# Optimization experiments

Measured on AMD Instinct MI355X. Metric: run time of the kernel, lower is better.

## Reference

```python
import jax, jax.numpy as jnp
import numpy as np
import math

B, S, D = 8, 4096, 768
H = 12
DH = D // H  # attention_head_size = 64


def setup_inputs() -> dict:
    key = jax.random.key(0)
    ks = jax.random.split(key, 6)
    sc = 0.02
    return {
        "hidden_states": jax.random.normal(ks[0], (B, S, D), dtype=jnp.float32),
        "attention_mask": jnp.zeros((B, 1, S), dtype=jnp.float32),
        "Wq": jax.random.normal(ks[1], (D, D), dtype=jnp.float32) * sc,
        "bq": jnp.zeros((D,), dtype=jnp.float32),
        "Wqa": jax.random.normal(ks[2], (H, D), dtype=jnp.float32) * sc,
        "bqa": jnp.zeros((H,), dtype=jnp.float32),
        "Wk": jax.random.normal(ks[3], (D, D), dtype=jnp.float32) * sc,
        "bk": jnp.zeros((D,), dtype=jnp.float32),
        "Wt": jax.random.normal(ks[4], (D, D), dtype=jnp.float32) * sc,
        "bt": jnp.zeros((D,), dtype=jnp.float32),
    }


def reference(hidden_states, attention_mask, Wq, bq, Wqa, bqa, Wk, bk, Wt, bt):
    inv_sqrt_dh = 1.0 / math.sqrt(DH)
    # projections (torch nn.Linear: x @ W.T + b)
    q = hidden_states @ Wq.T + bq            # [B,S,D]
    k = hidden_states @ Wk.T + bk            # [B,S,D]
    # query attention logits -> [B,H,S]
    qfs = jnp.swapaxes(q @ Wqa.T + bqa, 1, 2) * inv_sqrt_dh + attention_mask
    qw = jax.nn.softmax(qfs, axis=-1)        # [B,H,S]
    ql = jnp.swapaxes(q.reshape(B, S, H, DH), 1, 2)  # [B,H,S,DH]
    kl = jnp.swapaxes(k.reshape(B, S, H, DH), 1, 2)  # [B,H,S,DH]
    # global pooled query per head
    pooled_q = jnp.einsum('bhs,bhsd->bhd', qw, ql)   # [B,H,DH]
    # key attention over pooled query
    qks = jnp.einsum('bhsd,bhd->bhs', kl, pooled_q) * inv_sqrt_dh + attention_mask
    qkw = jax.nn.softmax(qks, axis=-1)       # [B,H,S]
    pooled_k = jnp.einsum('bhs,bhsd->bhd', qkw, kl)  # [B,H,DH]
    # gate query with pooled key, merge heads
    wv = pooled_k[:, :, None, :] * ql        # [B,H,S,DH]
    wv = jnp.swapaxes(wv, 1, 2).reshape(B, S, D)
    return wv @ Wt.T + bt + q
```

## Files before the change

### kernel.cpp

```cpp
#include <hip/hip_runtime.h>
#include <cstdint>
#include <cstddef>

#define S_LEN 4096
#define NB 8
#define NH 12
#define DMODEL 768
#define DHEAD 64
#define M_TOT (NB * S_LEN)
#define INV_SQRT_DH 0.125f
#define WSZ (DMODEL * DMODEL)

typedef __attribute__((ext_vector_type(4))) float f32x4;
typedef __attribute__((ext_vector_type(8))) short bf16x8;

__device__ inline float bf2f(unsigned short h) {
    union { unsigned int u; float f; } v; v.u = ((unsigned int)h) << 16; return v.f;
}
__device__ inline unsigned short f2bf(float f) {
    union { float f; unsigned int u; } v; v.f = f;
    unsigned int r = v.u + 0x7FFFu + ((v.u >> 16) & 1u);
    return (unsigned short)(r >> 16);
}

__device__ inline void gload_lds16(const unsigned short* gp, void* lp) {
    __builtin_amdgcn_global_load_lds((const __attribute__((address_space(1))) void*)gp,
                                     (__attribute__((address_space(3))) void*)lp,
                                     16, 0, 0);
}

__global__ void prep_all(const float* __restrict__ hs,
                         const float* __restrict__ Wq, const float* __restrict__ Wk,
                         const float* __restrict__ Wt, const float* __restrict__ Wqa,
                         const float* __restrict__ bq, const float* __restrict__ bk,
                         unsigned short* __restrict__ hs_bf,
                         unsigned short* __restrict__ Wqk_bf, unsigned short* __restrict__ Wt_bf,
                         unsigned short* __restrict__ Wqa_bf, float* __restrict__ bqk) {
    int bid = blockIdx.x;
    int t = threadIdx.x;
    if (bid < 24576) {
        int off = bid * 1024 + t * 4;
        float4 v = *(const float4*)(hs + off);
        ushort4 o;
        o.x = f2bf(v.x); o.y = f2bf(v.y); o.z = f2bf(v.z); o.w = f2bf(v.w);
        *(ushort4*)(hs_bf + off) = o;
        return;
    }
    bid -= 24576;
    if (bid < 1728) {
        const float* src = (bid < 576) ? Wq : ((bid < 1152) ? Wk : Wt);
        unsigned short* dst = (bid < 576) ? Wqk_bf : ((bid < 1152) ? (Wqk_bf + WSZ) : Wt_bf);
        int off = (bid % 576) * 1024 + t * 4;
        float4 v = *(const float4*)(src + off);
        ushort4 o;
        o.x = f2bf(v.x); o.y = f2bf(v.y); o.z = f2bf(v.z); o.w = f2bf(v.w);
        *(ushort4*)(dst + off) = o;
    } else if (bid < 1740) {
        int off = (bid - 1728) * 1024 + t * 4;
        int h = off / DMODEL;
        ushort4 o = {0, 0, 0, 0};
        if (h < NH) {
            float4 v = *(const float4*)(Wqa + off);
            o.x = f2bf(v.x); o.y = f2bf(v.y); o.z = f2bf(v.z); o.w = f2bf(v.w);
        }
        *(ushort4*)(Wqa_bf + off) = o;
    } else {
        int off = (bid - 1740) * 1024 + t * 4;
        if (off < 2 * DMODEL) {
            const float* src = (off < DMODEL) ? (bq + off) : (bk + off - DMODEL);
            *(float4*)(bqk + off) = *(const float4*)src;
        }
    }
}

#define PH_MID() do { __builtin_amdgcn_s_barrier(); \
    asm volatile("s_waitcnt lgkmcnt(0)"); \
    __builtin_amdgcn_sched_barrier(0); \
    __builtin_amdgcn_s_setprio(1); } while (0)
#define PH_END() do { __builtin_amdgcn_s_setprio(0); \
    __builtin_amdgcn_s_barrier(); } while (0)

#define STG_A(q, kt, BO) gload_lds16(pA + (size_t)((q) * 64) * 768 + (kt) * 64, \
                                     lds + (BO) + (q) * 8192 + wOff)
#define STG_B(q, kt, BO) gload_lds16(pB + (size_t)((q) * 64) * 768 + (kt) * 64, \
                                     lds + (BO) + 32768 + (q) * 8192 + wOff)

#define LD_A(mh, BO) do { _Pragma("unroll") for (int mm = 0; mm < 4; ++mm) { \
    a[mm][0] = *(const bf16x8*)(lds + (BO) + aRd0 + ((mh) * 4 + mm) * 2048); \
    a[mm][1] = *(const bf16x8*)(lds + (BO) + aRd1 + ((mh) * 4 + mm) * 2048); } } while (0)
#define LD_B(nh, BO) do { _Pragma("unroll") for (int nn = 0; nn < 2; ++nn) { \
    b[(nh) * 2 + nn][0] = *(const bf16x8*)(lds + (BO) + bRd0 + ((nh) * 2 + nn) * 2048); \
    b[(nh) * 2 + nn][1] = *(const bf16x8*)(lds + (BO) + bRd1 + ((nh) * 2 + nn) * 2048); } } while (0)
#define MFMAQ(mh, nh) do { _Pragma("unroll") for (int mm = 0; mm < 4; ++mm) \
    _Pragma("unroll") for (int nn = 0; nn < 2; ++nn) { \
        acc[(mh) * 4 + mm][(nh) * 2 + nn] = __builtin_amdgcn_mfma_f32_16x16x32_bf16( \
            a[mm][0], b[(nh) * 2 + nn][0], acc[(mh) * 4 + mm][(nh) * 2 + nn], 0, 0, 0); \
        acc[(mh) * 4 + mm][(nh) * 2 + nn] = __builtin_amdgcn_mfma_f32_16x16x32_bf16( \
            a[mm][1], b[(nh) * 2 + nn][1], acc[(mh) * 4 + mm][(nh) * 2 + nn], 0, 0, 0); } } while (0)

__global__ __launch_bounds__(512, 2) void gemm8(
    const unsigned short* __restrict__ A,
    const unsigned short* __restrict__ Bw,
    const float* __restrict__ bias,
    unsigned short* __restrict__ qOut,
    unsigned short* __restrict__ kOut,
    int ntn)
{
    __shared__ __align__(16) char lds[131072];

    int nwg = gridDim.x;
    int bid = blockIdx.x;
    int cpx = nwg >> 3;
    int swz = (bid & 7) * cpx + (bid >> 3);
    int bidn = swz % ntn, bidm = swz / ntn;
    int m0 = bidm * 256, n0 = bidn * 256;

    int t = threadIdx.x;
    int w = t >> 6, lane = t & 63;
    int lr = lane & 15, lk = lane >> 4;
    int wr = w >> 2, wc = w & 3;
    int wOff = w << 10;

    int srow = t >> 3;
    int sblk = (t & 7) ^ (srow & 7);
    const unsigned short* pA = A + (size_t)(m0 + srow) * 768 + sblk * 8;
    const unsigned short* pB = Bw + (size_t)(n0 + srow) * 768 + sblk * 8;

    int sx = lr & 7;
    int aRd0 = (wr * 128 + lr) * 128 + ((0 + lk) ^ sx) * 16;
    int aRd1 = (wr * 128 + lr) * 128 + ((4 + lk) ^ sx) * 16;
    int bRd0 = 32768 + (wc * 64 + lr) * 128 + ((0 + lk) ^ sx) * 16;
    int bRd1 = 32768 + (wc * 64 + lr) * 128 + ((4 + lk) ^ sx) * 16;

    f32x4 acc[8][4];
#pragma unroll
    for (int m = 0; m < 8; ++m)
#pragma unroll
        for (int n = 0; n < 4; ++n)
            acc[m][n] = (f32x4){0.f, 0.f, 0.f, 0.f};
    bf16x8 a[4][2], b[4][2];

    STG_A(0, 0, 0); STG_A(1, 0, 0); STG_A(2, 0, 0); STG_A(3, 0, 0);
    STG_B(0, 0, 0); STG_B(1, 0, 0); STG_B(2, 0, 0); STG_B(3, 0, 0);
    STG_A(0, 1, 65536); STG_A(2, 1, 65536);
    STG_B(0, 1, 65536); STG_B(1, 1, 65536); STG_B(2, 1, 65536); STG_B(3, 1, 65536);
    asm volatile("s_waitcnt vmcnt(6)");
    __builtin_amdgcn_s_barrier();

    for (int i = 0; i < 6; ++i) {
        int ktE = 2 * i, ktO = 2 * i + 1;
        int s2 = (i < 5);
        LD_A(0, 0); LD_B(0, 0);
        STG_A(1, ktO, 65536); STG_A(3, ktO, 65536);
        PH_MID(); MFMAQ(0, 0); PH_END();
        LD_B(1, 0);
        if (s2) { STG_A(0, ktE + 2, 0); STG_A(2, ktE + 2, 0); }
        PH_MID(); MFMAQ(0, 1); PH_END();
        LD_A(1, 0);
        if (s2) { STG_B(0, ktE + 2, 0); STG_B(1, ktE + 2, 0); }
        PH_MID(); MFMAQ(1, 1); PH_END();
        if (s2) { STG_B(2, ktE + 2, 0); STG_B(3, ktE + 2, 0); }
        PH_MID(); MFMAQ(1, 0);
        __builtin_amdgcn_s_setprio(0);
        if (s2) { asm volatile("s_waitcnt vmcnt(6)"); }
        else    { asm volatile("s_waitcnt vmcnt(0)"); }
        __builtin_amdgcn_s_barrier();
        LD_A(0, 65536); LD_B(0, 65536);
        if (s2) { STG_A(1, ktE + 2, 0); STG_A(3, ktE + 2, 0); }
        PH_MID(); MFMAQ(0, 0); PH_END();
        LD_B(1, 65536);
        if (s2) { STG_A(0, ktO + 2, 65536); STG_A(2, ktO + 2, 65536); }
        PH_MID(); MFMAQ(0, 1); PH_END();
        LD_A(1, 65536);
        if (s2) { STG_B(0, ktO + 2, 65536); STG_B(1, ktO + 2, 65536); }
        PH_MID(); MFMAQ(1, 1); PH_END();
        if (s2) { STG_B(2, ktO + 2, 65536); STG_B(3, ktO + 2, 65536); }
        PH_MID(); MFMAQ(1, 0);
        __builtin_amdgcn_s_setprio(0);
        if (s2) { asm volatile("s_waitcnt vmcnt(6)"); }
        __builtin_amdgcn_s_barrier();
    }

    unsigned short* outBf = (bidn < 3) ? qOut : kOut;
    int nc0 = (bidn < 3) ? n0 : (n0 - 768);
#pragma unroll
    for (int m = 0; m < 8; ++m) {
        int gr0 = m0 + wr * 128 + m * 16 + lk * 4;
#pragma unroll
        for (int n = 0; n < 4; ++n) {
            int gc = n0 + wc * 64 + n * 16 + lr;
            int oc = nc0 + wc * 64 + n * 16 + lr;
            float bv = bias[gc];
#pragma unroll
            for (int r = 0; r < 4; ++r) {
                int gr = gr0 + r;
                outBf[(size_t)gr * 768 + oc] = f2bf(acc[m][n][r] + bv);
            }
        }
    }
}

#define STG6_A(q, kt, SB) gload_lds16(pA + (size_t)((q) * 64) * 768 + (kt) * 64, \
                                      lds + (SB) + (q) * 8192 + wOff)
#define STG6_B(q, kt, SB) gload_lds16(pB + (size_t)((q) * 64) * 768 + (kt) * 64, \
                                      lds + (SB) + 32768 + (q) * 8192 + wOff)

__global__ __launch_bounds__(512, 2) void gemm3(
    const unsigned short* __restrict__ A,
    const unsigned short* __restrict__ W8,
    const float* __restrict__ bias,
    float* __restrict__ outF,
    const unsigned short* __restrict__ resid)
{
    __shared__ __align__(16) char lds[147456];

    int nwg = gridDim.x;
    int bid = blockIdx.x;
    int cpx = nwg >> 3;
    int swz = (bid & 7) * cpx + (bid >> 3);
    int bidn = swz % 6, bidm = swz / 6;
    int m0 = bidm * 256, n0 = bidn * 128;

    const unsigned short* Bw = W8 + (size_t)(m0 >> 12) * WSZ;

    int t = threadIdx.x;
    int w = t >> 6, lane = t & 63;
    int lr = lane & 15, lk = lane >> 4;
    int wr = w >> 1, wc = w & 1;
    int wOff = w << 10;

    int srow = t >> 3;
    int sblk = (t & 7) ^ (srow & 7);
    const unsigned short* pA = A + (size_t)(m0 + srow) * 768 + sblk * 8;
    const unsigned short* pB = Bw + (size_t)(n0 + srow) * 768 + sblk * 8;

    int sx = lr & 7;
    int aRd0 = (wr * 64 + lr) * 128 + ((0 + lk) ^ sx) * 16;
    int aRd1 = (wr * 64 + lr) * 128 + ((4 + lk) ^ sx) * 16;
    int bRd0 = 32768 + (wc * 64 + lr) * 128 + ((0 + lk) ^ sx) * 16;
    int bRd1 = 32768 + (wc * 64 + lr) * 128 + ((4 + lk) ^ sx) * 16;

    f32x4 acc[4][4];
#pragma unroll
    for (int m = 0; m < 4; ++m)
#pragma unroll
        for (int n = 0; n < 4; ++n)
            acc[m][n] = (f32x4){0.f, 0.f, 0.f, 0.f};
    bf16x8 a[4][2], b[4][2];

    STG6_A(0, 0, 0); STG6_A(1, 0, 0); STG6_A(2, 0, 0); STG6_A(3, 0, 0);
    STG6_B(0, 0, 0); STG6_B(1, 0, 0);
    STG6_A(0, 1, 49152); STG6_A(1, 1, 49152); STG6_A(2, 1, 49152); STG6_A(3, 1, 49152);
    STG6_B(0, 1, 49152); STG6_B(1, 1, 49152);
    asm volatile("s_waitcnt vmcnt(6)");
    __builtin_amdgcn_s_barrier();

#define TILE6(tt, BUF, SB) do { \
    if ((tt) <= 9) { STG6_A(0, (tt) + 2, SB); STG6_A(1, (tt) + 2, SB); \
                     STG6_A(2, (tt) + 2, SB); STG6_A(3, (tt) + 2, SB); \
                     STG6_B(0, (tt) + 2, SB); STG6_B(1, (tt) + 2, SB); } \
    _Pragma("unroll") for (int mm = 0; mm < 4; ++mm) { \
        a[mm][0] = *(const bf16x8*)(lds + (BUF) + aRd0 + mm * 2048); \
        a[mm][1] = *(const bf16x8*)(lds + (BUF) + aRd1 + mm * 2048); } \
    _Pragma("unroll") for (int nn = 0; nn < 4; ++nn) { \
        b[nn][0] = *(const bf16x8*)(lds + (BUF) + bRd0 + nn * 2048); \
        b[nn][1] = *(const bf16x8*)(lds + (BUF) + bRd1 + nn * 2048); } \
    PH_MID(); \
    _Pragma("unroll") for (int mm = 0; mm < 4; ++mm) \
    _Pragma("unroll") for (int nn = 0; nn < 4; ++nn) { \
        acc[mm][nn] = __builtin_amdgcn_mfma_f32_16x16x32_bf16(a[mm][0], b[nn][0], acc[mm][nn], 0, 0, 0); \
        acc[mm][nn] = __builtin_amdgcn_mfma_f32_16x16x32_bf16(a[mm][1], b[nn][1], acc[mm][nn], 0, 0, 0); } \
    __builtin_amdgcn_s_setprio(0); \
    if ((tt) <= 9)       { asm volatile("s_waitcnt vmcnt(6)"); } \
    else if ((tt) == 10) { asm volatile("s_waitcnt vmcnt(0)"); } \
    __builtin_amdgcn_s_barrier(); \
} while (0)

    for (int ii = 0; ii < 4; ++ii) {
        int tb = ii * 3;
        TILE6(tb + 0, 0,     98304);
        TILE6(tb + 1, 49152, 0);
        TILE6(tb + 2, 98304, 49152);
    }

#pragma unroll
    for (int m = 0; m < 4; ++m) {
        int gr0 = m0 + wr * 64 + m * 16 + lk * 4;
#pragma unroll
        for (int n = 0; n < 4; ++n) {
            int gc = n0 + wc * 64 + n * 16 + lr;
            float bv = bias[gc];
#pragma unroll
            for (int r = 0; r < 4; ++r) {
                int gr = gr0 + r;
                float v = acc[m][n][r] + bv + bf2f(resid[(size_t)gr * 768 + gc]);
                outF[(size_t)gr * DMODEL + gc] = v;
            }
        }
    }
}

__global__ __launch_bounds__(256) void qfs_kernel(
    const unsigned short* __restrict__ q,
    const unsigned short* __restrict__ wqa,
    const float* __restrict__ bqa,
    const float* __restrict__ mask,
    float* __restrict__ qfs)
{
    int t = threadIdx.x;
    int w = t >> 6, lane = t & 63;
    int lr = lane & 15, lk = lane >> 4;
    int m0 = blockIdx.x * 64 + w * 16;

    f32x4 acc = (f32x4){0.f, 0.f, 0.f, 0.f};
    for (int k0 = 0; k0 < DMODEL; k0 += 32) {
        bf16x8 av = *(const bf16x8*)&q[(size_t)(m0 + lr) * 768 + k0 + lk * 8];
        bf16x8 bv = *(const bf16x8*)&wqa[lr * DMODEL + k0 + lk * 8];
        acc = __builtin_amdgcn_mfma_f32_16x16x32_bf16(av, bv, acc, 0, 0, 0);
    }
    if (lr < NH) {
        float bv = bqa[lr];
#pragma unroll
        for (int r = 0; r < 4; ++r) {
            int m = m0 + lk * 4 + r;
            int b_ = m >> 12;
            int s = m & (S_LEN - 1);
            qfs[((size_t)b_ * NH + lr) * S_LEN + s] = acc[r] * INV_SQRT_DH + bv + mask[b_ * S_LEN + s];
        }
    }
}

__global__ __launch_bounds__(256) void pool1_kernel(
    const float* __restrict__ logits,
    const unsigned short* __restrict__ qc,
    float* __restrict__ parts)
{
    int bid = blockIdx.x;
    int bh = bid >> 3, c = bid & 7;
    int b = bh / NH, h = bh % NH;
    int s0 = c * 512;
    int t = threadIdx.x;

    __shared__ float w[512];
    __shared__ float red[8];
    __shared__ float part[4][64];

    const float* lg = logits + (size_t)bh * S_LEN + s0;
    float l0 = lg[t], l1 = lg[t + 256];
    float m = fmaxf(l0, l1);
#pragma unroll
    for (int off = 32; off; off >>= 1) m = fmaxf(m, __shfl_xor(m, off));
    if ((t & 63) == 0) red[t >> 6] = m;
    __syncthreads();
    float M = fmaxf(fmaxf(red[0], red[1]), fmaxf(red[2], red[3]));
    float w0 = __expf(l0 - M), w1 = __expf(l1 - M);
    w[t] = w0; w[t + 256] = w1;
    float z = w0 + w1;
#pragma unroll
    for (int off = 32; off; off >>= 1) z += __shfl_xor(z, off);
    if ((t & 63) == 0) red[4 + (t >> 6)] = z;
    __syncthreads();
    float Z = red[4] + red[5] + red[6] + red[7];

    int dblk = t & 7, rgrp = t >> 3;
    const unsigned short* xp = qc + ((size_t)(b * S_LEN + s0)) * 768 + h * DHEAD + dblk * 8;
    float acc[8];
#pragma unroll
    for (int e = 0; e < 8; ++e) acc[e] = 0.f;
    for (int j = 0; j < 16; ++j) {
        int r = j * 32 + rgrp;
        bf16x8 v = *(const bf16x8*)(xp + (size_t)r * 768);
        float wr = w[r];
#pragma unroll
        for (int e = 0; e < 8; ++e) acc[e] += wr * bf2f((unsigned short)v[e]);
    }
#pragma unroll
    for (int off = 8; off <= 32; off <<= 1)
#pragma unroll
        for (int e = 0; e < 8; ++e) acc[e] += __shfl_xor(acc[e], off);
    if ((t & 63) < 8) {
#pragma unroll
        for (int e = 0; e < 8; ++e) part[t >> 6][(t & 7) * 8 + e] = acc[e];
    }
    __syncthreads();
    float* dst = parts + ((size_t)bh * 8 + c) * 72;
    if (t < 64) dst[t] = part[0][t] + part[1][t] + part[2][t] + part[3][t];
    else if (t == 64) dst[64] = M;
    else if (t == 65) dst[65] = Z;
}

__global__ __launch_bounds__(256) void pool2_kernel(
    const float* __restrict__ parts1,
    const unsigned short* __restrict__ kc,
    const float* __restrict__ mask,
    float* __restrict__ parts2)
{
    int bid = blockIdx.x;
    int bh = bid >> 3, c = bid & 7;
    int b = bh / NH, h = bh % NH;
    int s0 = c * 512;
    int t = threadIdx.x;

    __shared__ float pq[64];
    __shared__ float w[512];
    __shared__ float red[8];
    __shared__ float part[4][64];

    if (t < 64) {
        const float* p1 = parts1 + (size_t)bh * 8 * 72;
        float M1 = -1e30f;
#pragma unroll
        for (int cc = 0; cc < 8; ++cc) M1 = fmaxf(M1, p1[cc * 72 + 64]);
        float Z1 = 0.f, a1 = 0.f;
#pragma unroll
        for (int cc = 0; cc < 8; ++cc) {
            float f = __expf(p1[cc * 72 + 64] - M1);
            Z1 += f * p1[cc * 72 + 65];
            a1 += f * p1[cc * 72 + t];
        }
        pq[t] = a1 / Z1;
    }
    __syncthreads();

    int dblk = t & 7, rgrp = t >> 3;
    float pq8[8];
#pragma unroll
    for (int e = 0; e < 8; ++e) pq8[e] = pq[dblk * 8 + e];

    const unsigned short* kp = kc + ((size_t)(b * S_LEN + s0)) * 768 + h * DHEAD + dblk * 8;

    for (int j = 0; j < 16; ++j) {
        int r = j * 32 + rgrp;
        bf16x8 v = *(const bf16x8*)(kp + (size_t)r * 768);
        float d = 0.f;
#pragma unroll
        for (int e = 0; e < 8; ++e) d += bf2f((unsigned short)v[e]) * pq8[e];
        d += __shfl_xor(d, 1); d += __shfl_xor(d, 2); d += __shfl_xor(d, 4);
        if (dblk == 0) w[r] = d * INV_SQRT_DH + mask[b * S_LEN + s0 + r];
    }
    __syncthreads();

    float l0 = w[t], l1 = w[t + 256];
    float m = fmaxf(l0, l1);
#pragma unroll
    for (int off = 32; off; off >>= 1) m = fmaxf(m, __shfl_xor(m, off));
    if ((t & 63) == 0) red[t >> 6] = m;
    __syncthreads();
    float M = fmaxf(fmaxf(red[0], red[1]), fmaxf(red[2], red[3]));
    float w0 = __expf(l0 - M), w1 = __expf(l1 - M);
    float z = w0 + w1;
#pragma unroll
    for (int off = 32; off; off >>= 1) z += __shfl_xor(z, off);
    if ((t & 63) == 0) red[4 + (t >> 6)] = z;
    __syncthreads();
    w[t] = w0; w[t + 256] = w1;
    __syncthreads();
    float Z = red[4] + red[5] + red[6] + red[7];

    float acc[8];
#pragma unroll
    for (int e = 0; e < 8; ++e) acc[e] = 0.f;
    for (int j = 0; j < 16; ++j) {
        int r = j * 32 + rgrp;
        bf16x8 v = *(const bf16x8*)(kp + (size_t)r * 768);
        float wr = w[r];
#pragma unroll
        for (int e = 0; e < 8; ++e) acc[e] += wr * bf2f((unsigned short)v[e]);
    }
#pragma unroll
    for (int off = 8; off <= 32; off <<= 1)
#pragma unroll
        for (int e = 0; e < 8; ++e) acc[e] += __shfl_xor(acc[e], off);
    if ((t & 63) < 8) {
#pragma unroll
        for (int e = 0; e < 8; ++e) part[t >> 6][(t & 7) * 8 + e] = acc[e];
    }
    __syncthreads();
    float* dst = parts2 + ((size_t)bh * 8 + c) * 72;
    if (t < 64) dst[t] = part[0][t] + part[1][t] + part[2][t] + part[3][t];
    else if (t == 64) dst[64] = M;
    else if (t == 65) dst[65] = Z;
}

__global__ __launch_bounds__(256) void gatedw_kernel(
    const float* __restrict__ parts2,
    const unsigned short* __restrict__ Wt_bf,
    unsigned short* __restrict__ W8)
{
    int bid = blockIdx.x;
    int b = bid / 96, rg = bid % 96;
    int t = threadIdx.x;

    __shared__ float mhc[96], Mh[12], fac[96], zh[12], pk[768];

    if (t < 96) mhc[t] = parts2[((size_t)(b * NH + t / 8) * 8 + (t & 7)) * 72 + 64];
    __syncthreads();
    if (t < 12) {
        float M = -1e30f;
#pragma unroll
        for (int cc = 0; cc < 8; ++cc) M = fmaxf(M, mhc[t * 8 + cc]);
        Mh[t] = M;
    }
    __syncthreads();
    if (t < 96) fac[t] = __expf(mhc[t] - Mh[t / 8]);
    __syncthreads();
    if (t < 12) {
        float Zm = 0.f;
#pragma unroll
        for (int cc = 0; cc < 8; ++cc)
            Zm += fac[t * 8 + cc] * parts2[((size_t)(b * NH + t) * 8 + cc) * 72 + 65];
        zh[t] = Zm;
    }
    __syncthreads();
#pragma unroll
    for (int j = 0; j < 3; ++j) {
        int col = t + 256 * j;
        int h = col >> 6, d = col & 63;
        const float* p2 = parts2 + (size_t)(b * NH + h) * 8 * 72;
        float v = 0.f;
#pragma unroll
        for (int cc = 0; cc < 8; ++cc) v += fac[h * 8 + cc] * p2[cc * 72 + d];
        pk[col] = v / zh[h];
    }
    __syncthreads();
#pragma unroll
    for (int j = 0; j < 3; ++j) {
        int idx = j * 2048 + t * 8;
        int r = rg * 8 + idx / DMODEL, k = idx % DMODEL;
        bf16x8 wv = *(const bf16x8*)(Wt_bf + (size_t)r * DMODEL + k);
        bf16x8 o;
#pragma unroll
        for (int e = 0; e < 8; ++e)
            o[e] = (short)f2bf(bf2f((unsigned short)wv[e]) * pk[k + e]);
        *(bf16x8*)(W8 + (size_t)b * WSZ + (size_t)r * DMODEL + k) = o;
    }
}

extern "C" void kernel_launch(void* const* d_in, const int* in_sizes, int n_in,
                              void* d_out, int out_size, void* d_ws, size_t ws_size,
                              hipStream_t stream) {
    const float* hs   = (const float*)d_in[0];
    const float* mask = (const float*)d_in[1];
    const float* Wq   = (const float*)d_in[2];
    const float* bq   = (const float*)d_in[3];
    const float* Wqa  = (const float*)d_in[4];
    const float* bqa  = (const float*)d_in[5];
    const float* Wk   = (const float*)d_in[6];
    const float* bk   = (const float*)d_in[7];
    const float* Wt   = (const float*)d_in[8];
    const float* bt   = (const float*)d_in[9];
    float* out = (float*)d_out;

    char* ws = (char*)d_ws;
    unsigned short* q_c    = (unsigned short*)(ws);
    unsigned short* k_c    = (unsigned short*)(ws + 50331648);
    unsigned short* hs_bf  = (unsigned short*)(ws + 100663296);
    unsigned short* W8     = hs_bf;
    unsigned short* Wqk_bf = (unsigned short*)(ws + 150994944);
    unsigned short* Wt_bf  = (unsigned short*)(ws + 153354240);
    unsigned short* Wqa_bf = (unsigned short*)(ws + 154533888);
    float* bqk    = (float*)(ws + 154558464);
    float* qfs    = (float*)(ws + 154564608);
    float* parts1 = (float*)(ws + 156137472);
    float* parts2 = (float*)(ws + 156358656);

    prep_all<<<26318, 256, 0, stream>>>(hs, Wq, Wk, Wt, Wqa, bq, bk,
                                        hs_bf, Wqk_bf, Wt_bf, Wqa_bf, bqk);

    gemm8<<<(M_TOT / 256) * 6, 512, 0, stream>>>(
        hs_bf, Wqk_bf, bqk, q_c, k_c, 6);

    qfs_kernel<<<M_TOT / 64, 256, 0, stream>>>(q_c, Wqa_bf, bqa, mask, qfs);
    pool1_kernel<<<NB * NH * 8, 256, 0, stream>>>(qfs, q_c, parts1);
    pool2_kernel<<<NB * NH * 8, 256, 0, stream>>>(parts1, k_c, mask, parts2);
    gatedw_kernel<<<NB * 96, 256, 0, stream>>>(parts2, Wt_bf, W8);

    gemm3<<<(M_TOT / 256) * 6, 512, 0, stream>>>(
        q_c, W8, bt, out, q_c);
}
```

Before: 212.4 us.

## Make GEMM kernels persistent over three output tiles with prefetch during epilogue

Both GEMM kernels now launch 256 workgroups instead of 768. Each workgroup loops over three consecutive N tiles for one M block, and it issues the first K-stage loads for the next tile before writing out the current tile's results. This is meant to cut launch and tail overhead and to hide each tile's prologue load latency behind the epilogue stores. In exchange there are fewer workgroups, which can reduce load balancing across CUs. The initial wait is also stricter (vmcnt(0)), and an extra barrier is added between tiles.

```diff
diff --git a/kernel.cpp b/kernel.cpp
--- a/kernel.cpp
+++ b/kernel.cpp
@@ -84,6 +84,11 @@
                                      lds + (BO) + (q) * 8192 + wOff)
 #define STG_B(q, kt, BO) gload_lds16(pB + (size_t)((q) * 64) * 768 + (kt) * 64, \
                                      lds + (BO) + 32768 + (q) * 8192 + wOff)
+#define STAGE14() do { \
+    STG_A(0, 0, 0); STG_A(1, 0, 0); STG_A(2, 0, 0); STG_A(3, 0, 0); \
+    STG_B(0, 0, 0); STG_B(1, 0, 0); STG_B(2, 0, 0); STG_B(3, 0, 0); \
+    STG_A(0, 1, 65536); STG_A(2, 1, 65536); \
+    STG_B(0, 1, 65536); STG_B(1, 1, 65536); STG_B(2, 1, 65536); STG_B(3, 1, 65536); } while (0)
 
 #define LD_A(mh, BO) do { _Pragma("unroll") for (int mm = 0; mm < 4; ++mm) { \
     a[mm][0] = *(const bf16x8*)(lds + (BO) + aRd0 + ((mh) * 4 + mm) * 2048); \
@@ -103,17 +108,14 @@
     const unsigned short* __restrict__ Bw,
     const float* __restrict__ bias,
     unsigned short* __restrict__ qOut,
-    unsigned short* __restrict__ kOut,
-    int ntn)
+    unsigned short* __restrict__ kOut)
 {
     __shared__ __align__(16) char lds[131072];
 
-    int nwg = gridDim.x;
     int bid = blockIdx.x;
-    int cpx = nwg >> 3;
-    int swz = (bid & 7) * cpx + (bid >> 3);
-    int bidn = swz % ntn, bidm = swz / ntn;
-    int m0 = bidm * 256, n0 = bidn * 256;
+    int swz = (bid & 7) * 32 + (bid >> 3);
+    int bidm = swz >> 1, half = swz & 1;
+    int m0 = bidm * 256;
 
     int t = threadIdx.x;
     int w = t >> 6, lane = t & 63;
@@ -124,7 +126,7 @@
     int srow = t >> 3;
     int sblk = (t & 7) ^ (srow & 7);
     const unsigned short* pA = A + (size_t)(m0 + srow) * 768 + sblk * 8;
-    const unsigned short* pB = Bw + (size_t)(n0 + srow) * 768 + sblk * 8;
+    unsigned short* outBf = half ? kOut : qOut;
 
     int sx = lr & 7;
     int aRd0 = (wr * 128 + lr) * 128 + ((0 + lk) ^ sx) * 16;
@@ -140,62 +142,81 @@
             acc[m][n] = (f32x4){0.f, 0.f, 0.f, 0.f};
     bf16x8 a[4][2], b[4][2];
 
-    STG_A(0, 0, 0); STG_A(1, 0, 0); STG_A(2, 0, 0); STG_A(3, 0, 0);
-    STG_B(0, 0, 0); STG_B(1, 0, 0); STG_B(2, 0, 0); STG_B(3, 0, 0);
-    STG_A(0, 1, 65536); STG_A(2, 1, 65536);
-    STG_B(0, 1, 65536); STG_B(1, 1, 65536); STG_B(2, 1, 65536); STG_B(3, 1, 65536);
-    asm volatile("s_waitcnt vmcnt(6)");
-    __builtin_amdgcn_s_barrier();
-
-    for (int i = 0; i < 6; ++i) {
-        int ktE = 2 * i, ktO = 2 * i + 1;
-        int s2 = (i < 5);
-        LD_A(0, 0); LD_B(0, 0);
-        STG_A(1, ktO, 65536); STG_A(3, ktO, 65536);
-        PH_MID(); MFMAQ(0, 0); PH_END();
-        LD_B(1, 0);
-        if (s2) { STG_A(0, ktE + 2, 0); STG_A(2, ktE + 2, 0); }
-        PH_MID(); MFMAQ(0, 1); PH_END();
-        LD_A(1, 0);
-        if (s2) { STG_B(0, ktE + 2, 0); STG_B(1, ktE + 2, 0); }
-        PH_MID(); MFMAQ(1, 1); PH_END();
-        if (s2) { STG_B(2, ktE + 2, 0); STG_B(3, ktE + 2, 0); }
-        PH_MID(); MFMAQ(1, 0);
-        __builtin_amdgcn_s_setprio(0);
-        if (s2) { asm volatile("s_waitcnt vmcnt(6)"); }
-        else    { asm volatile("s_waitcnt vmcnt(0)"); }
-        __builtin_amdgcn_s_barrier();
-        LD_A(0, 65536); LD_B(0, 65536);
-        if (s2) { STG_A(1, ktE + 2, 0); STG_A(3, ktE + 2, 0); }
-        PH_MID(); MFMAQ(0, 0); PH_END();
-        LD_B(1, 65536);
-        if (s2) { STG_A(0, ktO + 2, 65536); STG_A(2, ktO + 2, 65536); }
-        PH_MID(); MFMAQ(0, 1); PH_END();
-        LD_A(1, 65536);
-        if (s2) { STG_B(0, ktO + 2, 65536); STG_B(1, ktO + 2, 65536); }
-        PH_MID(); MFMAQ(1, 1); PH_END();
-        if (s2) { STG_B(2, ktO + 2, 65536); STG_B(3, ktO + 2, 65536); }
-        PH_MID(); MFMAQ(1, 0);
-        __builtin_amdgcn_s_setprio(0);
-        if (s2) { asm volatile("s_waitcnt vmcnt(6)"); }
-        __builtin_amdgcn_s_barrier();
-    }
-
-    unsigned short* outBf = (bidn < 3) ? qOut : kOut;
-    int nc0 = (bidn < 3) ? n0 : (n0 - 768);
-#pragma unroll
-    for (int m = 0; m < 8; ++m) {
-        int gr0 = m0 + wr * 128 + m * 16 + lk * 4;
-#pragma unroll
-        for (int n = 0; n < 4; ++n) {
-            int gc = n0 + wc * 64 + n * 16 + lr;
-            int oc = nc0 + wc * 64 + n * 16 + lr;
-            float bv = bias[gc];
-#pragma unroll
-            for (int r = 0; r < 4; ++r) {
-                int gr = gr0 + r;
-                outBf[(size_t)gr * 768 + oc] = f2bf(acc[m][n][r] + bv);
+    const unsigned short* pB;
+
+    for (int ot = 0; ot < 3; ++ot) {
+        int n0 = (half * 3 + ot) * 256;
+        if (ot == 0) {
+            pB = Bw + (size_t)(n0 + srow) * 768 + sblk * 8;
+            STAGE14();
+            asm volatile("s_waitcnt vmcnt(0)");
+            __builtin_amdgcn_s_barrier();
+        }
+
+        for (int i = 0; i < 6; ++i) {
+            int ktE = 2 * i, ktO = 2 * i + 1;
+            int s2 = (i < 5);
+            LD_A(0, 0); LD_B(0, 0);
+            STG_A(1, ktO, 65536); STG_A(3, ktO, 65536);
+            PH_MID(); MFMAQ(0, 0); PH_END();
+            LD_B(1, 0);
+            if (s2) { STG_A(0, ktE + 2, 0); STG_A(2, ktE + 2, 0); }
+            PH_MID(); MFMAQ(0, 1); PH_END();
+            LD_A(1, 0);
+            if (s2) { STG_B(0, ktE + 2, 0); STG_B(1, ktE + 2, 0); }
+            PH_MID(); MFMAQ(1, 1); PH_END();
+            if (s2) { STG_B(2, ktE + 2, 0); STG_B(3, ktE + 2, 0); }
+            PH_MID(); MFMAQ(1, 0);
+            __builtin_amdgcn_s_setprio(0);
+            if (s2) { asm volatile("s_waitcnt vmcnt(6)"); }
+            else    { asm volatile("s_waitcnt vmcnt(0)"); }
+            __builtin_amdgcn_s_barrier();
+            LD_A(0, 65536); LD_B(0, 65536);
+            if (s2) { STG_A(1, ktE + 2, 0); STG_A(3, ktE + 2, 0); }
+            PH_MID(); MFMAQ(0, 0); PH_END();
+            LD_B(1, 65536);
+            if (s2) { STG_A(0, ktO + 2, 65536); STG_A(2, ktO + 2, 65536); }
+            PH_MID(); MFMAQ(0, 1); PH_END();
+            LD_A(1, 65536);
+            if (s2) { STG_B(0, ktO + 2, 65536); STG_B(1, ktO + 2, 65536); }
+            PH_MID(); MFMAQ(1, 1); PH_END();
+            if (s2) { STG_B(2, ktO + 2, 65536); STG_B(3, ktO + 2, 65536); }
+            PH_MID(); MFMAQ(1, 0);
+            __builtin_amdgcn_s_setprio(0);
+            if (s2) { asm volatile("s_waitcnt vmcnt(6)"); }
+            __builtin_amdgcn_s_barrier();
+        }
+
+        if (ot < 2) {
+            pB = Bw + (size_t)(n0 + 256 + srow) * 768 + sblk * 8;
+            STAGE14();
+        }
+
+        int oc0 = ot * 256;
+#pragma unroll
+        for (int m = 0; m < 8; ++m) {
+            int gr0 = m0 + wr * 128 + m * 16 + lk * 4;
+#pragma unroll
+            for (int n = 0; n < 4; ++n) {
+                int gc = n0 + wc * 64 + n * 16 + lr;
+                int oc = oc0 + wc * 64 + n * 16 + lr;
+                float bv = bias[gc];
+#pragma unroll
+                for (int r = 0; r < 4; ++r) {
+                    int gr = gr0 + r;
+                    outBf[(size_t)gr * 768 + oc] = f2bf(acc[m][n][r] + bv);
+                }
             }
+        }
+
+        if (ot < 2) {
+#pragma unroll
+            for (int m = 0; m < 8; ++m)
+#pragma unroll
+                for (int n = 0; n < 4; ++n)
+                    acc[m][n] = (f32x4){0.f, 0.f, 0.f, 0.f};
+            asm volatile("s_waitcnt vmcnt(0)");
+            __builtin_amdgcn_s_barrier();
         }
     }
 }
@@ -204,56 +225,11 @@
                                       lds + (SB) + (q) * 8192 + wOff)
 #define STG6_B(q, kt, SB) gload_lds16(pB + (size_t)((q) * 64) * 768 + (kt) * 64, \
                                       lds + (SB) + 32768 + (q) * 8192 + wOff)
-
-__global__ __launch_bounds__(512, 2) void gemm3(
-    const unsigned short* __restrict__ A,
-    const unsigned short* __restrict__ W8,
-    const float* __restrict__ bias,
-    float* __restrict__ outF,
-    const unsigned short* __restrict__ resid)
-{
-    __shared__ __align__(16) char lds[147456];
-
-    int nwg = gridDim.x;
-    int bid = blockIdx.x;
-    int cpx = nwg >> 3;
-    int swz = (bid & 7) * cpx + (bid >> 3);
-    int bidn = swz % 6, bidm = swz / 6;
-    int m0 = bidm * 256, n0 = bidn * 128;
-
-    const unsigned short* Bw = W8 + (size_t)(m0 >> 12) * WSZ;
-
-    int t = threadIdx.x;
-    int w = t >> 6, lane = t & 63;
-    int lr = lane & 15, lk = lane >> 4;
-    int wr = w >> 1, wc = w & 1;
-    int wOff = w << 10;
-
-    int srow = t >> 3;
-    int sblk = (t & 7) ^ (srow & 7);
-    const unsigned short* pA = A + (size_t)(m0 + srow) * 768 + sblk * 8;
-    const unsigned short* pB = Bw + (size_t)(n0 + srow) * 768 + sblk * 8;
-
-    int sx = lr & 7;
-    int aRd0 = (wr * 64 + lr) * 128 + ((0 + lk) ^ sx) * 16;
-    int aRd1 = (wr * 64 + lr) * 128 + ((4 + lk) ^ sx) * 16;
-    int bRd0 = 32768 + (wc * 64 + lr) * 128 + ((0 + lk) ^ sx) * 16;
-    int bRd1 = 32768 + (wc * 64 + lr) * 128 + ((4 + lk) ^ sx) * 16;
-
-    f32x4 acc[4][4];
-#pragma unroll
-    for (int m = 0; m < 4; ++m)
-#pragma unroll
-        for (int n = 0; n < 4; ++n)
-            acc[m][n] = (f32x4){0.f, 0.f, 0.f, 0.f};
-    bf16x8 a[4][2], b[4][2];
-
-    STG6_A(0, 0, 0); STG6_A(1, 0, 0); STG6_A(2, 0, 0); STG6_A(3, 0, 0);
-    STG6_B(0, 0, 0); STG6_B(1, 0, 0);
-    STG6_A(0, 1, 49152); STG6_A(1, 1, 49152); STG6_A(2, 1, 49152); STG6_A(3, 1, 49152);
-    STG6_B(0, 1, 49152); STG6_B(1, 1, 49152);
-    asm volatile("s_waitcnt vmcnt(6)");
-    __builtin_amdgcn_s_barrier();
+#define STAGE12() do { \
+    STG6_A(0, 0, 0); STG6_A(1, 0, 0); STG6_A(2, 0, 0); STG6_A(3, 0, 0); \
+    STG6_B(0, 0, 0); STG6_B(1, 0, 0); \
+    STG6_A(0, 1, 49152); STG6_A(1, 1, 49152); STG6_A(2, 1, 49152); STG6_A(3, 1, 49152); \
+    STG6_B(0, 1, 49152); STG6_B(1, 1, 49152); } while (0)
 
 #define TILE6(tt, BUF, SB) do { \
     if ((tt) <= 9) { STG6_A(0, (tt) + 2, SB); STG6_A(1, (tt) + 2, SB); \
@@ -276,26 +252,93 @@
     __builtin_amdgcn_s_barrier(); \
 } while (0)
 
-    for (int ii = 0; ii < 4; ++ii) {
-        int tb = ii * 3;
-        TILE6(tb + 0, 0,     98304);
-        TILE6(tb + 1, 49152, 0);
-        TILE6(tb + 2, 98304, 49152);
-    }
-
-#pragma unroll
-    for (int m = 0; m < 4; ++m) {
-        int gr0 = m0 + wr * 64 + m * 16 + lk * 4;
-#pragma unroll
-        for (int n = 0; n < 4; ++n) {
-            int gc = n0 + wc * 64 + n * 16 + lr;
-            float bv = bias[gc];
-#pragma unroll
-            for (int r = 0; r < 4; ++r) {
-                int gr = gr0 + r;
-                float v = acc[m][n][r] + bv + bf2f(resid[(size_t)gr * 768 + gc]);
-                outF[(size_t)gr * DMODEL + gc] = v;
+__global__ __launch_bounds__(512, 2) void gemm3(
+    const unsigned short* __restrict__ A,
+    const unsigned short* __restrict__ W8,
+    const float* __restrict__ bias,
+    float* __restrict__ outF,
+    const unsigned short* __restrict__ resid)
+{
+    __shared__ __align__(16) char lds[147456];
+
+    int bid = blockIdx.x;
+    int swz = (bid & 7) * 32 + (bid >> 3);
+    int bidm = swz >> 1, half = swz & 1;
+    int m0 = bidm * 256;
+
+    const unsigned short* BwB = W8 + (size_t)(m0 >> 12) * WSZ;
+
+    int t = threadIdx.x;
+    int w = t >> 6, lane = t & 63;
+    int lr = lane & 15, lk = lane >> 4;
+    int wr = w >> 1, wc = w & 1;
+    int wOff = w << 10;
+
+    int srow = t >> 3;
+    int sblk = (t & 7) ^ (srow & 7);
+    const unsigned short* pA = A + (size_t)(m0 + srow) * 768 + sblk * 8;
+
+    int sx = lr & 7;
+    int aRd0 = (wr * 64 + lr) * 128 + ((0 + lk) ^ sx) * 16;
+    int aRd1 = (wr * 64 + lr) * 128 + ((4 + lk) ^ sx) * 16;
+    int bRd0 = 32768 + (wc * 64 + lr) * 128 + ((0 + lk) ^ sx) * 16;
+    int bRd1 = 32768 + (wc * 64 + lr) * 128 + ((4 + lk) ^ sx) * 16;
+
+    f32x4 acc[4][4];
+#pragma unroll
+    for (int m = 0; m < 4; ++m)
+#pragma unroll
+        for (int n = 0; n < 4; ++n)
+            acc[m][n] = (f32x4){0.f, 0.f, 0.f, 0.f};
+    bf16x8 a[4][2], b[4][2];
+
+    const unsigned short* pB;
+
+    for (int ot = 0; ot < 3; ++ot) {
+        int n0 = (half * 3 + ot) * 128;
+        if (ot == 0) {
+            pB = BwB + (size_t)(n0 + srow) * 768 + sblk * 8;
+            STAGE12();
+            asm volatile("s_waitcnt vmcnt(0)");
+            __builtin_amdgcn_s_barrier();
+        }
+
+        for (int ii = 0; ii < 4; ++ii) {
+            int tb = ii * 3;
+            TILE6(tb + 0, 0,     98304);
+            TILE6(tb + 1, 49152, 0);
+            TILE6(tb + 2, 98304, 49152);
+        }
+
+        if (ot < 2) {
+            pB = BwB + (size_t)(n0 + 128 + srow) * 768 + sblk * 8;
+            STAGE12();
+        }
+
+#pragma unroll
+        for (int m = 0; m < 4; ++m) {
+            int gr0 = m0 + wr * 64 + m * 16 + lk * 4;
+#pragma unroll
+            for (int n = 0; n < 4; ++n) {
+                int gc = n0 + wc * 64 + n * 16 + lr;
+                float bv = bias[gc];
+#pragma unroll
+                for (int r = 0; r < 4; ++r) {
+                    int gr = gr0 + r;
+                    float v = acc[m][n][r] + bv + bf2f(resid[(size_t)gr * 768 + gc]);
+                    outF[(size_t)gr * DMODEL + gc] = v;
+                }
             }
+        }
+
+        if (ot < 2) {
+#pragma unroll
+            for (int m = 0; m < 4; ++m)
+#pragma unroll
+                for (int n = 0; n < 4; ++n)
+                    acc[m][n] = (f32x4){0.f, 0.f, 0.f, 0.f};
+            asm volatile("s_waitcnt vmcnt(0)");
+            __builtin_amdgcn_s_barrier();
         }
     }
 }
@@ -567,14 +610,12 @@
     prep_all<<<26318, 256, 0, stream>>>(hs, Wq, Wk, Wt, Wqa, bq, bk,
                                         hs_bf, Wqk_bf, Wt_bf, Wqa_bf, bqk);
 
-    gemm8<<<(M_TOT / 256) * 6, 512, 0, stream>>>(
-        hs_bf, Wqk_bf, bqk, q_c, k_c, 6);
+    gemm8<<<256, 512, 0, stream>>>(hs_bf, Wqk_bf, bqk, q_c, k_c);
 
     qfs_kernel<<<M_TOT / 64, 256, 0, stream>>>(q_c, Wqa_bf, bqa, mask, qfs);
     pool1_kernel<<<NB * NH * 8, 256, 0, stream>>>(qfs, q_c, parts1);
     pool2_kernel<<<NB * NH * 8, 256, 0, stream>>>(parts1, k_c, mask, parts2);
     gatedw_kernel<<<NB * 96, 256, 0, stream>>>(parts2, Wt_bf, W8);
 
-    gemm3<<<(M_TOT / 256) * 6, 512, 0, stream>>>(
-        q_c, W8, bt, out, q_c);
-}
+    gemm3<<<256, 512, 0, stream>>>(q_c, W8, bt, out, q_c);
+}
```

Measured after the change: 283.4 us. +33.5%, slower.
